# Kernel optimization log

Hardware: AMD Instinct MI355X
Metric: run time of the kernel (lower is better)

Reference implementation:

```python
import jax, jax.numpy as jnp
import numpy as np
import math

B, C, N, M = 4, 128, 4096, 4096

def setup_inputs() -> dict:
    key = jax.random.key(0)
    ks = jax.random.split(key, 8)
    return {
        "x1": jax.random.normal(ks[0], (B, C, N), dtype=jnp.float32),
        "p1": jax.random.normal(ks[1], (B, 3, N), dtype=jnp.float32),
        "x2": jax.random.normal(ks[2], (B, C, M), dtype=jnp.float32),
        "p2": jax.random.normal(ks[3], (B, 3, M), dtype=jnp.float32),
        "Wq": jax.random.normal(ks[4], (C, C), dtype=jnp.float32) * 0.05,
        "Wk": jax.random.normal(ks[5], (C, C), dtype=jnp.float32) * 0.05,
        "Wv": jax.random.normal(ks[6], (C, C), dtype=jnp.float32) * 0.05,
        "Wpos": jax.random.normal(ks[7], (C, 3), dtype=jnp.float32) * 0.05,
    }

def reference(x1, p1, x2, p2, Wq, Wk, Wv, Wpos):
    # Conv1d with kernel_size=1, no bias == per-point matmul over channel dim.
    # NOTE: original forward uses self.pos for BOTH p1 and p2 (pos1 conv unused).
    pos = jnp.einsum('ck,bkn->bcn', Wpos, p1)   # [B,C,N]
    pos1 = jnp.einsum('ck,bkm->bcm', Wpos, p2)  # [B,C,M]
    q = jnp.einsum('dc,bcn->bdn', Wq, x1 + pos)   # [B,C,N]
    k = jnp.einsum('dc,bcm->bdm', Wk, x2 + pos1)  # [B,C,M]
    v = jnp.einsum('dc,bcm->bdm', Wv, x2)         # [B,C,M]
    scale = math.sqrt(q.shape[1])  # sqrt(C) -- q.shape[-2] in (B,C,N) layout
    energy = jnp.einsum('bcn,bcm->bnm', q, k) / scale  # [B,N,M]
    attention = jax.nn.softmax(energy, axis=-1)
    vout = jnp.einsum('bnm,bcm->bnc', attention, v)    # [B,N,C]
    out = jnp.swapaxes(vout, 1, 2) + x1                # [B,C,N] residual
    return jnp.swapaxes(out, 1, 2)                     # [B,N,C]
```

## Files before the change

### kernel.cpp

```cpp
#include <hip/hip_runtime.h>
#include <hip/hip_bf16.h>

#define B_ 4
#define C_ 128
#define N_ 4096
#define M_ 4096

typedef __bf16 bf16;
typedef __bf16 bf16x8 __attribute__((ext_vector_type(8)));
typedef float f32x4 __attribute__((ext_vector_type(4)));
typedef float f32x16 __attribute__((ext_vector_type(16)));

#define MFMA16(a, b, c) __builtin_amdgcn_mfma_f32_16x16x32_bf16(a, b, c, 0, 0, 0)
#define MFMA32(a, b, c) __builtin_amdgcn_mfma_f32_32x32x16_bf16(a, b, c, 0, 0, 0)

__device__ inline void gll16(const bf16* g, bf16* l) {
    __builtin_amdgcn_global_load_lds(
        (const __attribute__((address_space(1))) void*)g,
        (__attribute__((address_space(3))) void*)l, 16, 0, 0);
}

__device__ inline unsigned cvtpk(float a, float b) {
    unsigned r;
    asm("v_cvt_pk_bf16_f32 %0, %1, %2" : "=v"(r) : "v"(a), "v"(b));
    return r;
}

__global__ __launch_bounds__(256) void wcvt_kernel(
    const float* __restrict__ Wq, const float* __restrict__ Wk,
    const float* __restrict__ Wv, bf16* __restrict__ Wb) {
    int i = (blockIdx.x * 256 + threadIdx.x) * 4;
    const float* src = (i < 16384) ? Wq : (i < 32768) ? Wk : Wv;
    int off = i & 16383;
    float4 v = *(const float4*)(src + off);
    union { ushort4 u4; bf16 h[4]; } pk;
    pk.h[0] = (bf16)v.x; pk.h[1] = (bf16)v.y;
    pk.h[2] = (bf16)v.z; pk.h[3] = (bf16)v.w;
    *(ushort4*)(Wb + i) = pk.u4;
}

__global__ __launch_bounds__(768) void proj_kernel(
    const float* __restrict__ x1, const float* __restrict__ p1,
    const float* __restrict__ x2, const float* __restrict__ p2,
    const bf16* __restrict__ Wb, const float* __restrict__ Wpos,
    bf16* __restrict__ Qt, bf16* __restrict__ Kt, bf16* __restrict__ Vt) {
    __shared__ __align__(16) bf16 xbuf[3 * 64 * 136];
    bf16* xp1 = xbuf;
    bf16* xp2 = xbuf + 8704;
    bf16* xr2 = xbuf + 17408;
    __shared__ float pp1[3 * 64], pp2[3 * 64], wls[384];

    const int t = threadIdx.x;
    const int b = blockIdx.y;
    const int n0 = blockIdx.x * 64;

    if (t < 48) {
        int k3 = t / 16, i4 = (t & 15) * 4;
        *(float4*)&pp1[k3 * 64 + i4] = *(const float4*)(p1 + ((size_t)b * 3 + k3) * N_ + n0 + i4);
    } else if (t < 96) {
        int tt = t - 48;
        int k3 = tt / 16, i4 = (tt & 15) * 4;
        *(float4*)&pp2[k3 * 64 + i4] = *(const float4*)(p2 + ((size_t)b * 3 + k3) * N_ + n0 + i4);
    } else if (t < 192) {
        int i4 = (t - 96) * 4;
        *(float4*)&wls[i4] = *(const float4*)(Wpos + i4);
    }
    __syncthreads();

    for (int s = t; s < 2048; s += 768) {
        int c = s >> 4, n4 = (s & 15) * 4;
        float4 xv = *(const float4*)(x1 + ((size_t)b * C_ + c) * N_ + n0 + n4);
        float w0 = wls[c * 3 + 0], w1 = wls[c * 3 + 1], w2 = wls[c * 3 + 2];
        const float* xa = &xv.x;
        #pragma unroll
        for (int j = 0; j < 4; ++j) {
            float pos = w0 * pp1[n4 + j] + w1 * pp1[64 + n4 + j] + w2 * pp1[128 + n4 + j];
            xp1[(n4 + j) * 136 + c] = (bf16)(xa[j] + pos);
        }
    }
    for (int s = t; s < 2048; s += 768) {
        int c = s >> 4, n4 = (s & 15) * 4;
        float4 xv = *(const float4*)(x2 + ((size_t)b * C_ + c) * N_ + n0 + n4);
        float w0 = wls[c * 3 + 0], w1 = wls[c * 3 + 1], w2 = wls[c * 3 + 2];
        const float* xa = &xv.x;
        #pragma unroll
        for (int j = 0; j < 4; ++j) {
            float pos = w0 * pp2[n4 + j] + w1 * pp2[64 + n4 + j] + w2 * pp2[128 + n4 + j];
            xp2[(n4 + j) * 136 + c] = (bf16)(xa[j] + pos);
            xr2[(n4 + j) * 136 + c] = (bf16)xa[j];
        }
    }
    __syncthreads();

    const int w = t >> 6;
    const int lane = t & 63;
    const int col = lane & 15, quad = lane >> 4;
    const int role = w >> 2, band = w & 3;
    const int nl = band * 16 + col;
    const int n = n0 + nl;

    const bf16* src = (role == 0) ? xp1 : (role == 1) ? xp2 : xr2;
    const bf16* Wm = Wb + role * 16384;

    bf16x8 bx[4];
    #pragma unroll
    for (int cs = 0; cs < 4; ++cs)
        bx[cs] = *(const bf16x8*)&src[nl * 136 + cs * 32 + quad * 8];

    __syncthreads();
    bf16* vt = xbuf;

    #pragma unroll
    for (int dt = 0; dt < 8; ++dt) {
        f32x4 acc = {0.f, 0.f, 0.f, 0.f};
        #pragma unroll
        for (int cs = 0; cs < 4; ++cs) {
            bf16x8 wf = *(const bf16x8*)(Wm + (dt * 16 + col) * 128 + cs * 32 + quad * 8);
            acc = MFMA16(wf, bx[cs], acc);
        }
        if (role < 2) {
            bf16* Ot = (role == 0) ? Qt : Kt;
            union { ushort4 u4; bf16 h[4]; } pk;
            #pragma unroll
            for (int r = 0; r < 4; ++r) pk.h[r] = (bf16)acc[r];
            *(ushort4*)(Ot + ((size_t)b * N_ + n) * C_ + dt * 16 + quad * 4) = pk.u4;
        } else {
            #pragma unroll
            for (int r = 0; r < 4; ++r)
                vt[(dt * 16 + quad * 4 + r) * 72 + nl] = (bf16)acc[r];
        }
    }
    __syncthreads();

    for (int s = t; s < 1024; s += 768) {
        int c = s >> 3, off = s & 7;
        *(uint4*)(Vt + ((size_t)b * C_ + c) * (size_t)M_ + n0 + off * 8) =
            *(const uint4*)&vt[c * 72 + off * 8];
    }
}

__global__ __launch_bounds__(512) void attn_kernel(
    const bf16* __restrict__ Qt, const bf16* __restrict__ Kt,
    const bf16* __restrict__ Vt, const float* __restrict__ x1,
    float* __restrict__ out) {
    __shared__ __align__(16) char smem[132096];

    const int t = threadIdx.x;
    const int w = t >> 6;
    const int lane = t & 63;
    const int col = lane & 31;
    const int hi = lane >> 5;
    const int kg = w & 3;
    const int qg = w >> 2;

    const int g0 = blockIdx.x;
    const int xcd = g0 & 7;
    const int b = xcd >> 1;
    const int qt = (xcd & 1) + ((g0 >> 3) << 1);
    const int n0 = qt * 64;

    const float KS = 0.12752107168406815f;

    const bf16* Kbase = Kt + (size_t)b * M_ * C_;
    const bf16* Vbase = Vt + (size_t)b * C_ * M_;

    bf16x8 qf[8];
    {
        const bf16* Qb = Qt + ((size_t)b * N_ + n0 + qg * 32 + col) * C_ + hi * 8;
        #pragma unroll
        for (int cs = 0; cs < 8; ++cs)
            qf[cs] = *(const bf16x8*)(Qb + cs * 16);
    }

    f32x16 oacc[4];
    #pragma unroll
    for (int i = 0; i < 4; ++i)
        #pragma unroll
        for (int j = 0; j < 16; ++j) oacc[i][j] = 0.f;
    float lacc = 0.f;

    const int key_l = (kg << 5) + col;
    const int kxor = (key_l & 15) << 4;

    auto stageK = [&](int m0, char* dst) {
        #pragma unroll
        for (int i = 0; i < 4; ++i) {
            int g = ((w << 2) + i) * 64 + lane;
            int key = g >> 4;
            int sp = (g & 15) ^ (key & 15);
            gll16(Kbase + (size_t)(m0 + key) * C_ + sp * 8,
                  (bf16*)dst + ((w << 2) + i) * 512);
        }
    };
    auto stageV = [&](int m0, char* dst) {
        #pragma unroll
        for (int i = 0; i < 4; ++i) {
            int g = ((w << 2) + i) * 64 + lane;
            int c = g >> 4;
            int sp = (g & 15) ^ (c & 15);
            gll16(Vbase + (size_t)c * M_ + m0 + sp * 8,
                  (bf16*)dst + ((w << 2) + i) * 512);
        }
    };

    stageK(0, smem);
    stageV(0, smem + 65536);

    int buf = 0;
    for (int ch = 0; ch < 32; ++ch) {
        asm volatile("s_waitcnt vmcnt(0)" ::: "memory");
        __builtin_amdgcn_sched_barrier(0);
        __builtin_amdgcn_s_barrier();

        if (ch < 31) {
            stageK((ch + 1) << 7, smem + ((buf ^ 1) << 15));
            stageV((ch + 1) << 7, smem + 65536 + ((buf ^ 1) << 15));
        }

        const char* kbp = smem + (buf << 15) + key_l * 256;

        f32x16 s0a, s1a;
        #pragma unroll
        for (int j = 0; j < 16; ++j) { s0a[j] = 0.f; s1a[j] = 0.f; }
        __builtin_amdgcn_s_setprio(1);
        #pragma unroll
        for (int cs = 0; cs < 4; ++cs) {
            bf16x8 kf = *(const bf16x8*)(kbp + ((((cs << 1) + hi) << 4) ^ kxor));
            s0a = MFMA32(kf, qf[cs], s0a);
        }
        #pragma unroll
        for (int cs = 4; cs < 8; ++cs) {
            bf16x8 kf = *(const bf16x8*)(kbp + ((((cs << 1) + hi) << 4) ^ kxor));
            s1a = MFMA32(kf, qf[cs], s1a);
        }
        __builtin_amdgcn_s_setprio(0);

        float p[16];
        #pragma unroll
        for (int r = 0; r < 16; ++r) {
            float e = fminf((s0a[r] + s1a[r]) * KS, 60.f);
            p[r] = __builtin_amdgcn_exp2f(e);
        }
        {
            float s01 = (p[0] + p[1]) + (p[2] + p[3]);
            float s23 = (p[4] + p[5]) + (p[6] + p[7]);
            float s45 = (p[8] + p[9]) + (p[10] + p[11]);
            float s67 = (p[12] + p[13]) + (p[14] + p[15]);
            lacc += (s01 + s23) + (s45 + s67);
        }
        unsigned W0 = cvtpk(p[0], p[1]),  W1 = cvtpk(p[2], p[3]);
        unsigned W2 = cvtpk(p[4], p[5]),  W3 = cvtpk(p[6], p[7]);
        unsigned W4 = cvtpk(p[8], p[9]),  W5 = cvtpk(p[10], p[11]);
        unsigned W6 = cvtpk(p[12], p[13]), W7 = cvtpk(p[14], p[15]);
        unsigned X0 = hi ? W0 : W2, X1 = hi ? W1 : W3;
        unsigned Y0 = hi ? W4 : W6, Y1 = hi ? W5 : W7;
        X0 = __shfl_xor(X0, 32, 64);  X1 = __shfl_xor(X1, 32, 64);
        Y0 = __shfl_xor(Y0, 32, 64);  Y1 = __shfl_xor(Y1, 32, 64);
        uint4 u0, u1;
        u0.x = hi ? X0 : W0;  u0.y = hi ? X1 : W1;
        u0.z = hi ? W2 : X0;  u0.w = hi ? W3 : X1;
        u1.x = hi ? Y0 : W4;  u1.y = hi ? Y1 : W5;
        u1.z = hi ? W6 : Y0;  u1.w = hi ? W7 : Y1;
        bf16x8 af0 = __builtin_bit_cast(bf16x8, u0);
        bf16x8 af1 = __builtin_bit_cast(bf16x8, u1);

        const char* vbB = smem + 65536 + (buf << 15);
        __builtin_amdgcn_s_setprio(1);
        #pragma unroll
        for (int ct = 0; ct < 4; ++ct) {
            int c = (ct << 5) + col;
            const char* vbp = vbB + c * 256;
            int vxor = (c & 15) << 4;
            bf16x8 vf0 = *(const bf16x8*)(vbp + ((((kg << 2) + hi) << 4) ^ vxor));
            bf16x8 vf1 = *(const bf16x8*)(vbp + ((((kg << 2) + 2 + hi) << 4) ^ vxor));
            oacc[ct] = MFMA32(af0, vf0, oacc[ct]);
            oacc[ct] = MFMA32(af1, vf1, oacc[ct]);
        }
        __builtin_amdgcn_s_setprio(0);

        asm volatile("s_waitcnt lgkmcnt(0)" ::: "memory");
        __builtin_amdgcn_sched_barrier(0);
        buf ^= 1;
    }

    __builtin_amdgcn_s_barrier();

    float* obuf = (float*)smem;
    float* lps  = (float*)(smem + 131072);

    lacc += __shfl_xor(lacc, 32, 64);
    if (hi == 0) lps[(kg << 6) + (qg << 5) + col] = lacc;

    #pragma unroll
    for (int ct = 0; ct < 4; ++ct)
        #pragma unroll
        for (int r = 0; r < 16; ++r) {
            int q = (r & 3) + ((r >> 2) << 3) + (hi << 2);
            obuf[kg * 8192 + ((qg << 5) + q) * 128 + (ct << 5) + col] = oacc[ct][r];
        }
    __syncthreads();

    const int c2 = lane << 1;
    #pragma unroll
    for (int j = 0; j < 8; ++j) {
        int q = (w << 3) + j;
        float s0 = 0.f, s1 = 0.f;
        #pragma unroll
        for (int pp = 0; pp < 4; ++pp) {
            float2 v = *(const float2*)&obuf[pp * 8192 + q * 128 + c2];
            s0 += v.x; s1 += v.y;
        }
        float lsum = lps[q] + lps[64 + q] + lps[128 + q] + lps[192 + q];
        float linv = 1.0f / lsum;
        int n = n0 + q;
        float o0 = s0 * linv + x1[((size_t)b * C_ + c2) * N_ + n];
        float o1 = s1 * linv + x1[((size_t)b * C_ + c2 + 1) * N_ + n];
        *(float2*)&out[((size_t)b * N_ + n) * C_ + c2] = make_float2(o0, o1);
    }
}

extern "C" void kernel_launch(void* const* d_in, const int* in_sizes, int n_in,
                              void* d_out, int out_size, void* d_ws, size_t ws_size,
                              hipStream_t stream) {
    const float* x1   = (const float*)d_in[0];
    const float* p1   = (const float*)d_in[1];
    const float* x2   = (const float*)d_in[2];
    const float* p2   = (const float*)d_in[3];
    const float* Wq   = (const float*)d_in[4];
    const float* Wk   = (const float*)d_in[5];
    const float* Wv   = (const float*)d_in[6];
    const float* Wpos = (const float*)d_in[7];
    float* out = (float*)d_out;

    bf16* Qt = (bf16*)d_ws;
    bf16* Kt = Qt + (size_t)B_ * N_ * C_;
    bf16* Vt = Kt + (size_t)B_ * M_ * C_;

    bf16* Wb = (bf16*)d_out;

    wcvt_kernel<<<dim3(48), dim3(256), 0, stream>>>(Wq, Wk, Wv, Wb);
    proj_kernel<<<dim3(64, B_), dim3(768), 0, stream>>>(
        x1, p1, x2, p2, Wb, Wpos, Qt, Kt, Vt);
    attn_kernel<<<dim3(256), dim3(512), 0, stream>>>(Qt, Kt, Vt, x1, out);
}
```

Baseline: 146.3 us.

## Triple-buffer K tiles with partial vmcnt waits and write V directly from projection

The attention kernel now prefetches K two chunks ahead in a three-slot ring and keeps V double-buffered. It waits with vmcnt(4) rather than draining all loads, so the next chunk's loads stay in flight while the current chunk computes. This costs more LDS (160 KB), which may limit occupancy, and removes the per-iteration lgkmcnt wait. Separately, the projection kernel stores V transposed straight to global memory with scalar bf16 writes instead of staging through LDS. That drops two barriers but makes the V stores uncoalesced.

```diff
diff --git a/kernel.cpp b/kernel.cpp
--- a/kernel.cpp
+++ b/kernel.cpp
@@ -44,10 +44,9 @@
     const float* __restrict__ x2, const float* __restrict__ p2,
     const bf16* __restrict__ Wb, const float* __restrict__ Wpos,
     bf16* __restrict__ Qt, bf16* __restrict__ Kt, bf16* __restrict__ Vt) {
-    __shared__ __align__(16) bf16 xbuf[3 * 64 * 136];
-    bf16* xp1 = xbuf;
-    bf16* xp2 = xbuf + 8704;
-    bf16* xr2 = xbuf + 17408;
+    __shared__ __align__(16) bf16 xp1[64 * 136];
+    __shared__ __align__(16) bf16 xp2[64 * 136];
+    __shared__ __align__(16) bf16 xr2[64 * 136];
     __shared__ float pp1[3 * 64], pp2[3 * 64], wls[384];
 
     const int t = threadIdx.x;
@@ -107,9 +106,6 @@
     for (int cs = 0; cs < 4; ++cs)
         bx[cs] = *(const bf16x8*)&src[nl * 136 + cs * 32 + quad * 8];
 
-    __syncthreads();
-    bf16* vt = xbuf;
-
     #pragma unroll
     for (int dt = 0; dt < 8; ++dt) {
         f32x4 acc = {0.f, 0.f, 0.f, 0.f};
@@ -127,15 +123,8 @@
         } else {
             #pragma unroll
             for (int r = 0; r < 4; ++r)
-                vt[(dt * 16 + quad * 4 + r) * 72 + nl] = (bf16)acc[r];
-        }
-    }
-    __syncthreads();
-
-    for (int s = t; s < 1024; s += 768) {
-        int c = s >> 3, off = s & 7;
-        *(uint4*)(Vt + ((size_t)b * C_ + c) * (size_t)M_ + n0 + off * 8) =
-            *(const uint4*)&vt[c * 72 + off * 8];
+                Vt[((size_t)b * C_ + dt * 16 + quad * 4 + r) * (size_t)M_ + n] = (bf16)acc[r];
+        }
     }
 }
 
@@ -143,7 +132,7 @@
     const bf16* __restrict__ Qt, const bf16* __restrict__ Kt,
     const bf16* __restrict__ Vt, const float* __restrict__ x1,
     float* __restrict__ out) {
-    __shared__ __align__(16) char smem[132096];
+    __shared__ __align__(16) char smem[163840];
 
     const int t = threadIdx.x;
     const int w = t >> 6;
@@ -182,42 +171,46 @@
     const int key_l = (kg << 5) + col;
     const int kxor = (key_l & 15) << 4;
 
-    auto stageK = [&](int m0, char* dst) {
+    auto stageK = [&](int m0, int dstOff) {
         #pragma unroll
         for (int i = 0; i < 4; ++i) {
             int g = ((w << 2) + i) * 64 + lane;
             int key = g >> 4;
             int sp = (g & 15) ^ (key & 15);
             gll16(Kbase + (size_t)(m0 + key) * C_ + sp * 8,
-                  (bf16*)dst + ((w << 2) + i) * 512);
+                  (bf16*)(smem + dstOff) + ((w << 2) + i) * 512);
         }
     };
-    auto stageV = [&](int m0, char* dst) {
+    auto stageV = [&](int m0, int dstOff) {
         #pragma unroll
         for (int i = 0; i < 4; ++i) {
             int g = ((w << 2) + i) * 64 + lane;
             int c = g >> 4;
             int sp = (g & 15) ^ (c & 15);
             gll16(Vbase + (size_t)c * M_ + m0 + sp * 8,
-                  (bf16*)dst + ((w << 2) + i) * 512);
+                  (bf16*)(smem + dstOff) + ((w << 2) + i) * 512);
         }
     };
 
-    stageK(0, smem);
-    stageV(0, smem + 65536);
-
-    int buf = 0;
+    stageK(0, 0);
+    stageV(0, 98304);
+    stageK(128, 32768);
+
+    int koR = 0;
+    int koW = 65536;
+    int voR = 98304;
+
     for (int ch = 0; ch < 32; ++ch) {
-        asm volatile("s_waitcnt vmcnt(0)" ::: "memory");
+        if (ch < 31) asm volatile("s_waitcnt vmcnt(4)" ::: "memory");
+        else         asm volatile("s_waitcnt vmcnt(0)" ::: "memory");
         __builtin_amdgcn_sched_barrier(0);
         __builtin_amdgcn_s_barrier();
-
-        if (ch < 31) {
-            stageK((ch + 1) << 7, smem + ((buf ^ 1) << 15));
-            stageV((ch + 1) << 7, smem + 65536 + ((buf ^ 1) << 15));
-        }
-
-        const char* kbp = smem + (buf << 15) + key_l * 256;
+        __builtin_amdgcn_sched_barrier(0);
+
+        if (ch < 31) stageV((ch + 1) << 7, voR ^ 32768);
+        if (ch < 30) stageK((ch + 2) << 7, koW);
+
+        const char* kbp = smem + koR + key_l * 256;
 
         f32x16 s0a, s1a;
         #pragma unroll
@@ -264,7 +257,7 @@
         bf16x8 af0 = __builtin_bit_cast(bf16x8, u0);
         bf16x8 af1 = __builtin_bit_cast(bf16x8, u1);
 
-        const char* vbB = smem + 65536 + (buf << 15);
+        const char* vbB = smem + voR;
         __builtin_amdgcn_s_setprio(1);
         #pragma unroll
         for (int ct = 0; ct < 4; ++ct) {
@@ -278,11 +271,13 @@
         }
         __builtin_amdgcn_s_setprio(0);
 
-        asm volatile("s_waitcnt lgkmcnt(0)" ::: "memory");
-        __builtin_amdgcn_sched_barrier(0);
-        buf ^= 1;
-    }
-
+        koR += 32768; if (koR == 98304) koR = 0;
+        koW += 32768; if (koW == 98304) koW = 0;
+        voR ^= 32768;
+    }
+
+    asm volatile("s_waitcnt lgkmcnt(0)" ::: "memory");
+    __builtin_amdgcn_sched_barrier(0);
     __builtin_amdgcn_s_barrier();
 
     float* obuf = (float*)smem;
```

After: 145.2 us. About the same (-0.8%).
